# Optimization experiments

Measured on AMD Instinct MI355X. Metric: run time of the kernel, lower is better.

## Reference

```python
import jax, jax.numpy as jnp
import numpy as np

B, QL, HID = 4, 1, 4096
H, KVH, D = 16, 4, 256      # num_heads, num_kv_heads, head_dim
PAST = 8191
S = PAST + QL               # kv_seq_len = 8192
K_KEEP, R = 2048, 128       # heavy-hitter budget, channel top-r
THETA = 10000.0


def _rotate_half(x):
    return jnp.concatenate([-x[..., D // 2:], x[..., :D // 2]], axis=-1)


def _rope_tables(seq_len):
    inv_freq = 1.0 / (THETA ** (jnp.arange(0, D, 2, dtype=jnp.float32) / D))
    t = jnp.arange(seq_len, dtype=jnp.float32)
    freqs = jnp.outer(t, inv_freq)
    emb = jnp.concatenate([freqs, freqs], axis=-1)  # [S, D]
    return jnp.cos(emb), jnp.sin(emb)


def setup_inputs() -> dict:
    key = jax.random.key(0)
    ks = jax.random.split(key, 8)
    w = 0.02
    return {
        "hidden_states": jax.random.normal(ks[0], (B, QL, HID), jnp.float32),
        "attention_mask": jnp.zeros((B, 1, QL, S), jnp.float32),
        "position_ids": jnp.full((B, QL), PAST, jnp.int32),
        "past_key": jax.random.normal(ks[1], (B, KVH, PAST, D), jnp.float32),
        "past_value": jax.random.normal(ks[2], (B, KVH, PAST, D), jnp.float32),
        "Wq": w * jax.random.normal(ks[3], (H * D, HID), jnp.float32),
        "Wk": w * jax.random.normal(ks[4], (KVH * D, HID), jnp.float32),
        "Wv": w * jax.random.normal(ks[5], (KVH * D, HID), jnp.float32),
        "Wo": w * jax.random.normal(ks[6], (HID, H * D), jnp.float32),
    }


def reference(hidden_states, attention_mask, position_ids, past_key, past_value, Wq, Wk, Wv, Wo):
    b, q_len, _ = hidden_states.shape
    # QKV projections (no bias)
    q = (hidden_states @ Wq.T).reshape(b, q_len, H, D).transpose(0, 2, 1, 3)    # [b,H,q,D]
    k = (hidden_states @ Wk.T).reshape(b, q_len, KVH, D).transpose(0, 2, 1, 3)  # [b,KVH,q,D]
    v = (hidden_states @ Wv.T).reshape(b, q_len, KVH, D).transpose(0, 2, 1, 3)

    # RoPE at the current positions
    cos_t, sin_t = _rope_tables(S)
    cos = cos_t[position_ids][:, None]  # [b,1,q,D]
    sin = sin_t[position_ids][:, None]
    q = q * cos + _rotate_half(q) * sin
    k = k * cos + _rotate_half(k) * sin

    # append to KV cache, then GQA repeat (repeat_interleave over head dim)
    key = jnp.concatenate([past_key, k], axis=2)      # [b,KVH,S,D]
    value = jnp.concatenate([past_value, v], axis=2)
    n_rep = H // KVH
    key_r = jnp.repeat(key, n_rep, axis=1)            # [b,H,S,D]
    value_r = jnp.repeat(value, n_rep, axis=1)

    # --- heavy-hitter approximate scores: top-r channels of |q| ---
    i1 = jax.lax.top_k(jnp.abs(q), R)[1]                                   # [b,H,q,R]
    Q_hat = jnp.take_along_axis(q, i1, axis=-1)                            # [b,H,q,R]
    K_hat = jnp.take_along_axis(key_r, jnp.broadcast_to(i1, (b, H, S, R)), axis=-1)  # [b,H,S,R]
    scale = jnp.sqrt(D * jnp.abs(Q_hat).sum(-1, keepdims=True)
                     / jnp.abs(q).sum(-1, keepdims=True))                  # [b,H,q,1]
    s_hat = jax.nn.softmax(jnp.einsum('bhqr,bhsr->bhqs', Q_hat, K_hat) / scale
                           + attention_mask, axis=-1)                      # [b,H,q,S]

    # --- evict all but the top-k heavy hitters (rank of s_hat, descending) ---
    ranks = jnp.argsort(jnp.argsort(-s_hat, axis=-1), axis=-1)             # [b,H,q,S]
    aw = jnp.einsum('bhqd,bhsd->bhqs', q, key_r) / np.sqrt(D).astype(np.float32)
    aw = jnp.where(ranks >= K_KEEP, -jnp.inf, aw) + attention_mask
    probs = jax.nn.softmax(aw, axis=-1)
    y = jnp.einsum('bhqs,bhsd->bhqd', probs, value_r)                      # [b,H,q,D]

    out = y.transpose(0, 2, 1, 3).reshape(b, q_len, H * D) @ Wo.T          # [b,q,HID]
    return out
```

## Files before the change

### kernel.cpp

```cpp
#include <hip/hip_runtime.h>
#include <cmath>

#define B_   4
#define H_   16
#define KVH_ 4
#define D_   256
#define HID_ 4096
#define PAST_ 8191
#define S_   8192
#define KKEEP_ 2048
#define R_   128

#define OFF_Q     0
#define OFF_KN    16384
#define OFF_VN    20480
#define OFF_SCALE 24576
#define OFF_CMASK 24640
#define OFF_F     32768
#define OFF_A     557056
#define OFF_P     1081344
#define OFF_YP    1605632
#define OFF_Y     2654208

__global__ __launch_bounds__(256) void k1_qkv(
    const float* __restrict__ hidden, const int* __restrict__ pos_ids,
    const float* __restrict__ Wq, const float* __restrict__ Wk, const float* __restrict__ Wv,
    float* __restrict__ q_ws, float* __restrict__ knew, float* __restrict__ vnew)
{
    int slot = blockIdx.x >> 7;
    int d    = blockIdx.x & 127;
    const float* W; float* outp; int head; bool rope; int bstride;
    if (slot < 16)      { W = Wq; head = slot;      outp = q_ws + head * D_; rope = true;  bstride = H_ * D_; }
    else if (slot < 20) { W = Wk; head = slot - 16; outp = knew + head * D_; rope = true;  bstride = KVH_ * D_; }
    else                { W = Wv; head = slot - 20; outp = vnew + head * D_; rope = false; bstride = KVH_ * D_; }

    int rowbase = head * D_ + d;
    const float* w0 = W + (size_t)rowbase * HID_;
    const float* w1 = W + (size_t)(rowbase + 128) * HID_;

    float acc0[4] = {0.f, 0.f, 0.f, 0.f};
    float acc1[4] = {0.f, 0.f, 0.f, 0.f};
#pragma unroll
    for (int i = 0; i < 4; ++i) {
        int c = (threadIdx.x + 256 * i) * 4;
        float4 a0 = *(const float4*)(w0 + c);
        float4 a1 = *(const float4*)(w1 + c);
#pragma unroll
        for (int b = 0; b < 4; ++b) {
            float4 hv = *(const float4*)(hidden + b * HID_ + c);
            acc0[b] += a0.x * hv.x + a0.y * hv.y + a0.z * hv.z + a0.w * hv.w;
            acc1[b] += a1.x * hv.x + a1.y * hv.y + a1.z * hv.z + a1.w * hv.w;
        }
    }
#pragma unroll
    for (int off = 1; off < 64; off <<= 1) {
#pragma unroll
        for (int b = 0; b < 4; ++b) {
            acc0[b] += __shfl_xor(acc0[b], off, 64);
            acc1[b] += __shfl_xor(acc1[b], off, 64);
        }
    }
    __shared__ float red[4][8];
    int wv = threadIdx.x >> 6, ln = threadIdx.x & 63;
    if (ln == 0) {
#pragma unroll
        for (int b = 0; b < 4; ++b) { red[wv][b] = acc0[b]; red[wv][4 + b] = acc1[b]; }
    }
    __syncthreads();
    if (threadIdx.x == 0) {
        float x = (float)d * (1.0f / 128.0f);
        float invf = 1.0f / powf(10000.0f, x);
        for (int b = 0; b < 4; ++b) {
            float s0 = red[0][b] + red[1][b] + red[2][b] + red[3][b];
            float s1 = red[0][4 + b] + red[1][4 + b] + red[2][4 + b] + red[3][4 + b];
            float o0, o1;
            if (rope) {
                float ang = (float)pos_ids[b] * invf;
                double ad = (double)ang;
                float c = (float)cos(ad), sn = (float)sin(ad);
                o0 = s0 * c - s1 * sn;
                o1 = s1 * c + s0 * sn;
            } else { o0 = s0; o1 = s1; }
            outp[b * bstride + d]       = o0;
            outp[b * bstride + d + 128] = o1;
        }
    }
}

__global__ __launch_bounds__(256) void k1b_chan(
    const float* __restrict__ q_ws, float* __restrict__ scale_ws, unsigned* __restrict__ cmask_ws)
{
    int bh = blockIdx.x;
    int t  = threadIdx.x;
    __shared__ unsigned ua[256];
    __shared__ float red[256];
    __shared__ unsigned bm[8];
    __shared__ float s_all;

    float qv = q_ws[bh * 256 + t];
    float aq = fabsf(qv);
    ua[t] = __float_as_uint(aq);
    if (t < 8) bm[t] = 0u;
    __syncthreads();

    unsigned mine = ua[t];
    int rank = 0;
    for (int i = 0; i < 256; ++i) {
        unsigned o = ua[i];
        rank += (o > mine) || (o == mine && i < t);
    }
    bool kept = rank < R_;
    if (kept) atomicOr(&bm[t >> 5], 1u << (t & 31));

    red[t] = aq; __syncthreads();
    for (int off = 128; off; off >>= 1) { if (t < off) red[t] += red[t + off]; __syncthreads(); }
    if (t == 0) s_all = red[0];
    __syncthreads();
    red[t] = kept ? aq : 0.f; __syncthreads();
    for (int off = 128; off; off >>= 1) { if (t < off) red[t] += red[t + off]; __syncthreads(); }
    if (t == 0) scale_ws[bh] = sqrtf(256.0f * red[0] / s_all);
    if (t < 8) cmask_ws[bh * 8 + t] = bm[t];
}

__global__ __launch_bounds__(256) void k2_scores(
    const float* __restrict__ past_key, const float* __restrict__ knew,
    const float* __restrict__ q_ws, const float* __restrict__ scale_ws,
    const unsigned* __restrict__ cmask_ws, const float* __restrict__ amask,
    float* __restrict__ fsc, float* __restrict__ asc)
{
    int bkv   = blockIdx.x >> 7;
    int chunk = blockIdx.x & 127;
    int b = bkv >> 2, kvh = bkv & 3;
    int w = threadIdx.x >> 6, lane = threadIdx.x & 63;
    int g = lane >> 4, m = lane & 15;
    int h = kvh * 4 + g;

    const float* qp = q_ws + (b * H_ + h) * D_;
    const unsigned* cm = cmask_ws + (b * H_ + h) * 8;
    float inv_scale = 1.0f / scale_ws[b * H_ + h];

    float qr[16], ar[16];
#pragma unroll
    for (int i = 0; i < 4; ++i)
#pragma unroll
        for (int t = 0; t < 4; ++t) {
            int c = i * 64 + m * 4 + t;
            float q = qp[c];
            qr[i * 4 + t] = q;
            ar[i * 4 + t] = ((cm[c >> 5] >> (c & 31)) & 1u) ? q : 0.f;
        }

    const float* kbase = past_key + (size_t)(b * KVH_ + kvh) * PAST_ * D_;
    const float* knrow = knew + (b * KVH_ + kvh) * D_;
    float* fout = fsc + (size_t)(b * H_ + h) * S_;
    float* aout = asc + (size_t)(b * H_ + h) * S_;
    const float* mrow = amask + b * S_;
    int s0 = chunk * 64 + w * 16;

    const float* rA = (s0     < PAST_) ? (kbase + (size_t)s0 * D_)       : knrow;
    const float* rB = (s0 + 1 < PAST_) ? (kbase + (size_t)(s0 + 1) * D_) : knrow;
    float4 nA0 = *(const float4*)(rA + m * 4);
    float4 nA1 = *(const float4*)(rA + 64 + m * 4);
    float4 nA2 = *(const float4*)(rA + 128 + m * 4);
    float4 nA3 = *(const float4*)(rA + 192 + m * 4);
    float4 nB0 = *(const float4*)(rB + m * 4);
    float4 nB1 = *(const float4*)(rB + 64 + m * 4);
    float4 nB2 = *(const float4*)(rB + 128 + m * 4);
    float4 nB3 = *(const float4*)(rB + 192 + m * 4);

    for (int it = 0; it < 8; ++it) {
        int sA = s0 + 2 * it;
        float4 cA0 = nA0, cA1 = nA1, cA2 = nA2, cA3 = nA3;
        float4 cB0 = nB0, cB1 = nB1, cB2 = nB2, cB3 = nB3;
        if (it < 7) {
            int sn = sA + 2;
            const float* pA = (sn     < PAST_) ? (kbase + (size_t)sn * D_)       : knrow;
            const float* pB = (sn + 1 < PAST_) ? (kbase + (size_t)(sn + 1) * D_) : knrow;
            nA0 = *(const float4*)(pA + m * 4);
            nA1 = *(const float4*)(pA + 64 + m * 4);
            nA2 = *(const float4*)(pA + 128 + m * 4);
            nA3 = *(const float4*)(pA + 192 + m * 4);
            nB0 = *(const float4*)(pB + m * 4);
            nB1 = *(const float4*)(pB + 64 + m * 4);
            nB2 = *(const float4*)(pB + 128 + m * 4);
            nB3 = *(const float4*)(pB + 192 + m * 4);
        }
        float fullA = 0.f, apprA = 0.f, fullB = 0.f, apprB = 0.f;
        fullA += qr[0]*cA0.x + qr[1]*cA0.y + qr[2]*cA0.z + qr[3]*cA0.w;
        apprA += ar[0]*cA0.x + ar[1]*cA0.y + ar[2]*cA0.z + ar[3]*cA0.w;
        fullA += qr[4]*cA1.x + qr[5]*cA1.y + qr[6]*cA1.z + qr[7]*cA1.w;
        apprA += ar[4]*cA1.x + ar[5]*cA1.y + ar[6]*cA1.z + ar[7]*cA1.w;
        fullA += qr[8]*cA2.x + qr[9]*cA2.y + qr[10]*cA2.z + qr[11]*cA2.w;
        apprA += ar[8]*cA2.x + ar[9]*cA2.y + ar[10]*cA2.z + ar[11]*cA2.w;
        fullA += qr[12]*cA3.x + qr[13]*cA3.y + qr[14]*cA3.z + qr[15]*cA3.w;
        apprA += ar[12]*cA3.x + ar[13]*cA3.y + ar[14]*cA3.z + ar[15]*cA3.w;
        fullB += qr[0]*cB0.x + qr[1]*cB0.y + qr[2]*cB0.z + qr[3]*cB0.w;
        apprB += ar[0]*cB0.x + ar[1]*cB0.y + ar[2]*cB0.z + ar[3]*cB0.w;
        fullB += qr[4]*cB1.x + qr[5]*cB1.y + qr[6]*cB1.z + qr[7]*cB1.w;
        apprB += ar[4]*cB1.x + ar[5]*cB1.y + ar[6]*cB1.z + ar[7]*cB1.w;
        fullB += qr[8]*cB2.x + qr[9]*cB2.y + qr[10]*cB2.z + qr[11]*cB2.w;
        apprB += ar[8]*cB2.x + ar[9]*cB2.y + ar[10]*cB2.z + ar[11]*cB2.w;
        fullB += qr[12]*cB3.x + qr[13]*cB3.y + qr[14]*cB3.z + qr[15]*cB3.w;
        apprB += ar[12]*cB3.x + ar[13]*cB3.y + ar[14]*cB3.z + ar[15]*cB3.w;
#pragma unroll
        for (int off = 1; off < 16; off <<= 1) {
            fullA += __shfl_xor(fullA, off, 64);
            apprA += __shfl_xor(apprA, off, 64);
            fullB += __shfl_xor(fullB, off, 64);
            apprB += __shfl_xor(apprB, off, 64);
        }
        float2 mv = *(const float2*)(mrow + sA);
        if (m == 0) {
            float2 o; o.x = fullA * 0.0625f + mv.x; o.y = fullB * 0.0625f + mv.y;
            *(float2*)(fout + sA) = o;
        } else if (m == 1) {
            float2 o; o.x = apprA * inv_scale + mv.x; o.y = apprB * inv_scale + mv.y;
            *(float2*)(aout + sA) = o;
        }
    }
}

#define PAD(s) ((s) + ((s) >> 5))
__global__ __launch_bounds__(1024) void k3_select(
    const float* __restrict__ fsc, const float* __restrict__ asc, float* __restrict__ probs)
{
    int bh = blockIdx.x;
    int t  = threadIdx.x;
    int lane = t & 63, wid = t >> 6;
    __shared__ unsigned ua[8448];
    __shared__ unsigned hist2[16 * 257];
    __shared__ unsigned hist[256];
    __shared__ unsigned sf[256];
    __shared__ int wsum[16], wbase[16];
    __shared__ float wred[16];
    __shared__ unsigned sh_bin; __shared__ int sh_rem;
    __shared__ float sh_M, sh_Z;

    const float* ap = asc + (size_t)bh * S_;
    const float* fp = fsc + (size_t)bh * S_;

#pragma unroll
    for (int i = 0; i < 8; ++i) {
        int s = i * 1024 + t;
        unsigned u = __float_as_uint(ap[s]);
        u ^= (u & 0x80000000u) ? 0xFFFFFFFFu : 0x80000000u;
        ua[PAD(s)] = u;
    }

    unsigned prefix = 0; int rem = KKEEP_;
    for (int pass = 0; pass < 4; ++pass) {
        const int shift = 24 - 8 * pass;
        for (int j = t; j < 16 * 257; j += 1024) hist2[j] = 0;
        __syncthreads();
#pragma unroll
        for (int i = 0; i < 8; ++i) {
            unsigned u = ua[PAD(i * 1024 + t)];
            bool match = (pass == 0) || ((u >> (shift + 8)) == prefix);
            if (match) atomicAdd(&hist2[wid * 257 + ((u >> shift) & 255u)], 1u);
        }
        __syncthreads();
        if (t < 256) {
            unsigned hsum = 0;
#pragma unroll
            for (int w2 = 0; w2 < 16; ++w2) hsum += hist2[w2 * 257 + t];
            hist[t] = hsum;
        }
        __syncthreads();
        if (t < 64) {
            unsigned h0 = hist[t*4], h1 = hist[t*4+1], h2 = hist[t*4+2], h3 = hist[t*4+3];
            unsigned loc = h0 + h1 + h2 + h3;
            unsigned run = loc;
#pragma unroll
            for (int off = 1; off < 64; off <<= 1) {
                unsigned v = __shfl_down(run, off, 64);
                if (t + off < 64) run += v;
            }
            unsigned tail = run - loc;
            sf[t*4+3] = tail + h3;
            sf[t*4+2] = tail + h3 + h2;
            sf[t*4+1] = tail + h3 + h2 + h1;
            sf[t*4+0] = tail + loc;
        }
        __syncthreads();
        if (t < 256) {
            unsigned above = (t == 255) ? 0u : sf[t + 1];
            if (sf[t] >= (unsigned)rem && above < (unsigned)rem) {
                sh_bin = (unsigned)t;
                sh_rem = rem - (int)above;
            }
        }
        __syncthreads();
        prefix = (prefix << 8) | sh_bin;
        rem = sh_rem;
        __syncthreads();
    }
    unsigned ut = prefix; int Need = rem;

    int cnt = 0;
#pragma unroll
    for (int i = 0; i < 8; ++i)
        cnt += (ua[PAD(t * 8 + i)] == ut) ? 1 : 0;
    int inc = cnt;
#pragma unroll
    for (int off = 1; off < 64; off <<= 1) {
        int v = __shfl_up(inc, off, 64);
        if (lane >= off) inc += v;
    }
    if (lane == 63) wsum[wid] = inc;
    __syncthreads();
    if (t == 0) {
        int run = 0;
#pragma unroll
        for (int j = 0; j < 16; ++j) { int c = wsum[j]; wbase[j] = run; run += c; }
    }
    __syncthreads();
    int eqb = wbase[wid] + inc - cnt;
#pragma unroll
    for (int i = 0; i < 8; ++i) {
        int s = t * 8 + i;
        if (ua[PAD(s)] == ut) {
            ua[PAD(s)] = (eqb < Need) ? 0xFFFFFFFFu : 0u;
            ++eqb;
        }
    }
    __syncthreads();

    float m = -3.4e38f, z = 0.f;
#pragma unroll
    for (int i = 0; i < 8; ++i) {
        int s = i * 1024 + t;
        if (ua[PAD(s)] > ut) {
            float f = fp[s];
            if (f > m) { z = z * expf(m - f) + 1.f; m = f; }
            else       { z += expf(f - m); }
        }
    }
    float wm = m;
#pragma unroll
    for (int off = 1; off < 64; off <<= 1) wm = fmaxf(wm, __shfl_xor(wm, off, 64));
    if (lane == 0) wred[wid] = wm;
    __syncthreads();
    if (t == 0) {
        float M = wred[0];
#pragma unroll
        for (int j = 1; j < 16; ++j) M = fmaxf(M, wred[j]);
        sh_M = M;
    }
    __syncthreads();
    float M = sh_M;
    float zs = z * expf(m - M);
#pragma unroll
    for (int off = 1; off < 64; off <<= 1) zs += __shfl_xor(zs, off, 64);
    if (lane == 0) wred[wid] = zs;
    __syncthreads();
    if (t == 0) {
        float Z = 0.f;
#pragma unroll
        for (int j = 0; j < 16; ++j) Z += wred[j];
        sh_Z = Z;
    }
    __syncthreads();
    float invZ = 1.0f / sh_Z;

    float* pp = probs + (size_t)bh * S_;
#pragma unroll
    for (int i = 0; i < 8; ++i) {
        int s = i * 1024 + t;
        pp[s] = (ua[PAD(s)] > ut) ? expf(fp[s] - M) * invZ : 0.f;
    }
}

__global__ __launch_bounds__(256) void k4_wv(
    const float* __restrict__ past_value, const float* __restrict__ vnew,
    const float* __restrict__ probs, float* __restrict__ ypart)
{
    int bkv = blockIdx.x >> 6, chunk = blockIdx.x & 63;
    int b = bkv >> 2, kvh = bkv & 3;
    int w = threadIdx.x >> 6, lane = threadIdx.x & 63;
    int h0 = kvh * 4;

    const float* p0 = probs + (size_t)(b * H_ + h0) * S_;
    const float* vbase = past_value + (size_t)(b * KVH_ + kvh) * PAST_ * D_;
    const float* vnrow = vnew + (b * KVH_ + kvh) * D_;

    float acc[4][4] = {{0.f}};
    int s0 = chunk * 128 + w * 32;

    const float* rA = (s0     < PAST_) ? (vbase + (size_t)s0 * D_)       : vnrow;
    const float* rB = (s0 + 1 < PAST_) ? (vbase + (size_t)(s0 + 1) * D_) : vnrow;
    float4 vnA = *(const float4*)(rA + lane * 4);
    float4 vnB = *(const float4*)(rB + lane * 4);
    float2 pn0 = *(const float2*)(p0 + s0);
    float2 pn1 = *(const float2*)(p0 + S_ + s0);
    float2 pn2 = *(const float2*)(p0 + 2 * S_ + s0);
    float2 pn3 = *(const float2*)(p0 + 3 * S_ + s0);

    for (int it = 0; it < 16; ++it) {
        float4 vA = vnA, vB = vnB;
        float2 c0 = pn0, c1 = pn1, c2 = pn2, c3 = pn3;
        if (it < 15) {
            int sn = s0 + 2 * it + 2;
            const float* pA = (sn     < PAST_) ? (vbase + (size_t)sn * D_)       : vnrow;
            const float* pB = (sn + 1 < PAST_) ? (vbase + (size_t)(sn + 1) * D_) : vnrow;
            vnA = *(const float4*)(pA + lane * 4);
            vnB = *(const float4*)(pB + lane * 4);
            pn0 = *(const float2*)(p0 + sn);
            pn1 = *(const float2*)(p0 + S_ + sn);
            pn2 = *(const float2*)(p0 + 2 * S_ + sn);
            pn3 = *(const float2*)(p0 + 3 * S_ + sn);
        }
        acc[0][0] += c0.x * vA.x + c0.y * vB.x;
        acc[0][1] += c0.x * vA.y + c0.y * vB.y;
        acc[0][2] += c0.x * vA.z + c0.y * vB.z;
        acc[0][3] += c0.x * vA.w + c0.y * vB.w;
        acc[1][0] += c1.x * vA.x + c1.y * vB.x;
        acc[1][1] += c1.x * vA.y + c1.y * vB.y;
        acc[1][2] += c1.x * vA.z + c1.y * vB.z;
        acc[1][3] += c1.x * vA.w + c1.y * vB.w;
        acc[2][0] += c2.x * vA.x + c2.y * vB.x;
        acc[2][1] += c2.x * vA.y + c2.y * vB.y;
        acc[2][2] += c2.x * vA.z + c2.y * vB.z;
        acc[2][3] += c2.x * vA.w + c2.y * vB.w;
        acc[3][0] += c3.x * vA.x + c3.y * vB.x;
        acc[3][1] += c3.x * vA.y + c3.y * vB.y;
        acc[3][2] += c3.x * vA.z + c3.y * vB.z;
        acc[3][3] += c3.x * vA.w + c3.y * vB.w;
    }

    __shared__ float part[4][4][256];
#pragma unroll
    for (int j = 0; j < 4; ++j)
#pragma unroll
        for (int t4 = 0; t4 < 4; ++t4)
            part[w][j][lane * 4 + t4] = acc[j][t4];
    __syncthreads();

    float* yo = ypart + (size_t)(chunk * 16 + bkv) * 1024;
    for (int o = threadIdx.x; o < 1024; o += 256) {
        int j = o >> 8, d = o & 255;
        yo[o] = part[0][j][d] + part[1][j][d] + part[2][j][d] + part[3][j][d];
    }
}

__global__ __launch_bounds__(256) void k5_reduce(const float* __restrict__ ypart, float* __restrict__ yflat)
{
    int bh = blockIdx.x; int b = bh >> 4, h = bh & 15;
    int kvh = h >> 2, j = h & 3;
    int d = threadIdx.x;
    int bkv = b * 4 + kvh;
    float sum = 0.f;
    for (int c = 0; c < 64; ++c)
        sum += ypart[(size_t)(c * 16 + bkv) * 1024 + j * 256 + d];
    yflat[b * 4096 + h * 256 + d] = sum;
}

__global__ __launch_bounds__(256) void k6_out(
    const float* __restrict__ Wo, const float* __restrict__ yflat, float* __restrict__ out)
{
    int i = blockIdx.x;
    const float* wrow = Wo + (size_t)i * HID_;
    float acc[4] = {0.f, 0.f, 0.f, 0.f};
#pragma unroll
    for (int ii = 0; ii < 4; ++ii) {
        int c = (threadIdx.x + 256 * ii) * 4;
        float4 wv = *(const float4*)(wrow + c);
#pragma unroll
        for (int b = 0; b < 4; ++b) {
            float4 yv = *(const float4*)(yflat + b * 4096 + c);
            acc[b] += wv.x * yv.x + wv.y * yv.y + wv.z * yv.z + wv.w * yv.w;
        }
    }
#pragma unroll
    for (int off = 1; off < 64; off <<= 1)
#pragma unroll
        for (int b = 0; b < 4; ++b) acc[b] += __shfl_xor(acc[b], off, 64);
    __shared__ float red[4][4];
    int wv_ = threadIdx.x >> 6, ln = threadIdx.x & 63;
    if (ln == 0)
#pragma unroll
        for (int b = 0; b < 4; ++b) red[wv_][b] = acc[b];
    __syncthreads();
    if (threadIdx.x < 4) {
        int b = threadIdx.x;
        out[b * HID_ + i] = red[0][b] + red[1][b] + red[2][b] + red[3][b];
    }
}

extern "C" void kernel_launch(void* const* d_in, const int* in_sizes, int n_in,
                              void* d_out, int out_size, void* d_ws, size_t ws_size,
                              hipStream_t stream)
{
    const float* hidden = (const float*)d_in[0];
    const float* amask  = (const float*)d_in[1];
    const int*   posids = (const int*)d_in[2];
    const float* pkey   = (const float*)d_in[3];
    const float* pval   = (const float*)d_in[4];
    const float* Wq     = (const float*)d_in[5];
    const float* Wk     = (const float*)d_in[6];
    const float* Wv     = (const float*)d_in[7];
    const float* Wo     = (const float*)d_in[8];
    float* out = (float*)d_out;
    float* ws  = (float*)d_ws;

    float* q_ws   = ws + OFF_Q;
    float* knew   = ws + OFF_KN;
    float* vnew   = ws + OFF_VN;
    float* scale  = ws + OFF_SCALE;
    unsigned* cmask = (unsigned*)(ws + OFF_CMASK);
    float* fsc    = ws + OFF_F;
    float* asc    = ws + OFF_A;
    float* probs  = ws + OFF_P;
    float* ypart  = ws + OFF_YP;
    float* yflat  = ws + OFF_Y;

    k1_qkv  <<<dim3(3072), dim3(256), 0, stream>>>(hidden, posids, Wq, Wk, Wv, q_ws, knew, vnew);
    k1b_chan<<<dim3(64),   dim3(256), 0, stream>>>(q_ws, scale, cmask);
    k2_scores<<<dim3(2048), dim3(256), 0, stream>>>(pkey, knew, q_ws, scale, cmask, amask, fsc, asc);
    k3_select<<<dim3(64),  dim3(1024), 0, stream>>>(fsc, asc, probs);
    k4_wv   <<<dim3(1024), dim3(256), 0, stream>>>(pval, vnew, probs, ypart);
    k5_reduce<<<dim3(64),  dim3(256), 0, stream>>>(ypart, yflat);
    k6_out  <<<dim3(4096), dim3(256), 0, stream>>>(Wo, yflat, out);
}
```

Measured before the change: 427.2 us.

## Gather only kept value rows via compacted index list; precompute RoPE table

The select kernel now writes a per-head bitmask of kept positions. A new compaction kernel unions the masks across the four query heads that share a KV head, builds a prefix-summed index list and compacted probabilities, and pads both to multiples of 128. The weighted-V kernel and the reduce then cover only the compacted rows, skipping value rows whose probability is zero in all four heads. RoPE cos/sin values move out of the per-block QKV path into a tiny separate kernel, at the cost of two extra launches and scattered row gathers.

```diff
diff --git a/kernel.cpp b/kernel.cpp
--- a/kernel.cpp
+++ b/kernel.cpp
@@ -16,14 +16,32 @@
 #define OFF_VN    20480
 #define OFF_SCALE 24576
 #define OFF_CMASK 24640
-#define OFF_F     32768
-#define OFF_A     557056
-#define OFF_P     1081344
-#define OFF_YP    1605632
-#define OFF_Y     2654208
+#define OFF_ROPE  25152
+#define OFF_KBM   26176
+#define OFF_CNT   42560
+#define OFF_F     43008
+#define OFF_A     567296
+#define OFF_P     1091584
+#define OFF_YP    1615872
+#define OFF_PC    OFF_F
+#define OFF_LIST  OFF_A
+#define OFF_Y     OFF_KBM
+
+__global__ __launch_bounds__(256) void k0_rope(const int* __restrict__ pos_ids, float* __restrict__ ropet)
+{
+    for (int e = threadIdx.x; e < 512; e += 256) {
+        int b = e >> 7, d = e & 127;
+        float x = (float)d * (1.0f / 128.0f);
+        float invf = 1.0f / powf(10000.0f, x);
+        float ang = (float)pos_ids[b] * invf;
+        double ad = (double)ang;
+        ropet[e * 2]     = (float)cos(ad);
+        ropet[e * 2 + 1] = (float)sin(ad);
+    }
+}
 
 __global__ __launch_bounds__(256) void k1_qkv(
-    const float* __restrict__ hidden, const int* __restrict__ pos_ids,
+    const float* __restrict__ hidden, const float* __restrict__ ropet,
     const float* __restrict__ Wq, const float* __restrict__ Wk, const float* __restrict__ Wv,
     float* __restrict__ q_ws, float* __restrict__ knew, float* __restrict__ vnew)
 {
@@ -68,16 +86,13 @@
     }
     __syncthreads();
     if (threadIdx.x == 0) {
-        float x = (float)d * (1.0f / 128.0f);
-        float invf = 1.0f / powf(10000.0f, x);
         for (int b = 0; b < 4; ++b) {
             float s0 = red[0][b] + red[1][b] + red[2][b] + red[3][b];
             float s1 = red[0][4 + b] + red[1][4 + b] + red[2][4 + b] + red[3][4 + b];
             float o0, o1;
             if (rope) {
-                float ang = (float)pos_ids[b] * invf;
-                double ad = (double)ang;
-                float c = (float)cos(ad), sn = (float)sin(ad);
+                float c  = ropet[(b * 128 + d) * 2];
+                float sn = ropet[(b * 128 + d) * 2 + 1];
                 o0 = s0 * c - s1 * sn;
                 o1 = s1 * c + s0 * sn;
             } else { o0 = s0; o1 = s1; }
@@ -222,7 +237,8 @@
 
 #define PAD(s) ((s) + ((s) >> 5))
 __global__ __launch_bounds__(1024) void k3_select(
-    const float* __restrict__ fsc, const float* __restrict__ asc, float* __restrict__ probs)
+    const float* __restrict__ fsc, const float* __restrict__ asc,
+    float* __restrict__ probs, unsigned* __restrict__ kbm)
 {
     int bh = blockIdx.x;
     int t  = threadIdx.x;
@@ -363,51 +379,110 @@
     float invZ = 1.0f / sh_Z;
 
     float* pp = probs + (size_t)bh * S_;
+    unsigned* kb = kbm + bh * 256;
 #pragma unroll
     for (int i = 0; i < 8; ++i) {
         int s = i * 1024 + t;
-        pp[s] = (ua[PAD(s)] > ut) ? expf(fp[s] - M) * invZ : 0.f;
-    }
+        bool kp = ua[PAD(s)] > ut;
+        pp[s] = kp ? expf(fp[s] - M) * invZ : 0.f;
+        unsigned long long bal = __ballot(kp);
+        if (lane == 0) {
+            int wd = s >> 5;
+            kb[wd]     = (unsigned)bal;
+            kb[wd + 1] = (unsigned)(bal >> 32);
+        }
+    }
+}
+
+__global__ __launch_bounds__(256) void k3b_compact(
+    const unsigned* __restrict__ kbm, const float* __restrict__ probs,
+    int* __restrict__ counts, int* __restrict__ lst, float* __restrict__ pc)
+{
+    int g = blockIdx.x;
+    int t = threadIdx.x;
+    __shared__ int sc[256];
+
+    unsigned m0 = kbm[(g * 4 + 0) * 256 + t];
+    unsigned m1 = kbm[(g * 4 + 1) * 256 + t];
+    unsigned m2 = kbm[(g * 4 + 2) * 256 + t];
+    unsigned m3 = kbm[(g * 4 + 3) * 256 + t];
+    unsigned u = m0 | m1 | m2 | m3;
+    int cnt = __popc(u);
+    sc[t] = cnt; __syncthreads();
+    for (int off = 1; off < 256; off <<= 1) {
+        int v = (t >= off) ? sc[t - off] : 0;
+        __syncthreads();
+        sc[t] += v;
+        __syncthreads();
+    }
+    int base = sc[t] - cnt;
+    int total = sc[255];
+
+    const float* p0 = probs + (size_t)(g * 4) * S_;
+    int* lg = lst + g * 8192;
+    float* pg = pc + (size_t)g * 4 * 8192;
+#pragma unroll
+    for (int bit = 0; bit < 32; ++bit) {
+        if ((u >> bit) & 1u) {
+            int row = t * 32 + bit;
+            int pos = base + __popc(u & ((1u << bit) - 1u));
+            lg[pos] = row;
+            pg[pos]         = ((m0 >> bit) & 1u) ? p0[row]          : 0.f;
+            pg[8192 + pos]  = ((m1 >> bit) & 1u) ? p0[S_ + row]     : 0.f;
+            pg[16384 + pos] = ((m2 >> bit) & 1u) ? p0[2 * S_ + row] : 0.f;
+            pg[24576 + pos] = ((m3 >> bit) & 1u) ? p0[3 * S_ + row] : 0.f;
+        }
+    }
+    int pad_end = (total + 127) & ~127;
+    for (int p = total + t; p < pad_end; p += 256) {
+        lg[p] = PAST_;
+        pg[p] = 0.f; pg[8192 + p] = 0.f; pg[16384 + p] = 0.f; pg[24576 + p] = 0.f;
+    }
+    if (t == 0) counts[g] = total;
 }
 
 __global__ __launch_bounds__(256) void k4_wv(
     const float* __restrict__ past_value, const float* __restrict__ vnew,
-    const float* __restrict__ probs, float* __restrict__ ypart)
+    const int* __restrict__ counts, const int* __restrict__ lst,
+    const float* __restrict__ pc, float* __restrict__ ypart)
 {
     int bkv = blockIdx.x >> 6, chunk = blockIdx.x & 63;
+    int pad_end = (counts[bkv] + 127) & ~127;
+    if (chunk * 128 >= pad_end) return;
     int b = bkv >> 2, kvh = bkv & 3;
     int w = threadIdx.x >> 6, lane = threadIdx.x & 63;
-    int h0 = kvh * 4;
-
-    const float* p0 = probs + (size_t)(b * H_ + h0) * S_;
+
     const float* vbase = past_value + (size_t)(b * KVH_ + kvh) * PAST_ * D_;
     const float* vnrow = vnew + (b * KVH_ + kvh) * D_;
+    const int* lw = lst + bkv * 8192 + chunk * 128 + w * 32;
+    const float* pw = pc + (size_t)bkv * 4 * 8192 + chunk * 128 + w * 32;
 
     float acc[4][4] = {{0.f}};
-    int s0 = chunk * 128 + w * 32;
-
-    const float* rA = (s0     < PAST_) ? (vbase + (size_t)s0 * D_)       : vnrow;
-    const float* rB = (s0 + 1 < PAST_) ? (vbase + (size_t)(s0 + 1) * D_) : vnrow;
-    float4 vnA = *(const float4*)(rA + lane * 4);
-    float4 vnB = *(const float4*)(rB + lane * 4);
-    float2 pn0 = *(const float2*)(p0 + s0);
-    float2 pn1 = *(const float2*)(p0 + S_ + s0);
-    float2 pn2 = *(const float2*)(p0 + 2 * S_ + s0);
-    float2 pn3 = *(const float2*)(p0 + 3 * S_ + s0);
+
+    int rA = lw[0], rB = lw[1];
+    const float* prA = (rA < PAST_) ? (vbase + (size_t)rA * D_) : vnrow;
+    const float* prB = (rB < PAST_) ? (vbase + (size_t)rB * D_) : vnrow;
+    float4 vnA = *(const float4*)(prA + lane * 4);
+    float4 vnB = *(const float4*)(prB + lane * 4);
+    float2 pn0 = *(const float2*)(pw);
+    float2 pn1 = *(const float2*)(pw + 8192);
+    float2 pn2 = *(const float2*)(pw + 16384);
+    float2 pn3 = *(const float2*)(pw + 24576);
 
     for (int it = 0; it < 16; ++it) {
         float4 vA = vnA, vB = vnB;
         float2 c0 = pn0, c1 = pn1, c2 = pn2, c3 = pn3;
         if (it < 15) {
-            int sn = s0 + 2 * it + 2;
-            const float* pA = (sn     < PAST_) ? (vbase + (size_t)sn * D_)       : vnrow;
-            const float* pB = (sn + 1 < PAST_) ? (vbase + (size_t)(sn + 1) * D_) : vnrow;
+            int p2 = 2 * it + 2;
+            int rA2 = lw[p2], rB2 = lw[p2 + 1];
+            const float* pA = (rA2 < PAST_) ? (vbase + (size_t)rA2 * D_) : vnrow;
+            const float* pB = (rB2 < PAST_) ? (vbase + (size_t)rB2 * D_) : vnrow;
             vnA = *(const float4*)(pA + lane * 4);
             vnB = *(const float4*)(pB + lane * 4);
-            pn0 = *(const float2*)(p0 + sn);
-            pn1 = *(const float2*)(p0 + S_ + sn);
-            pn2 = *(const float2*)(p0 + 2 * S_ + sn);
-            pn3 = *(const float2*)(p0 + 3 * S_ + sn);
+            pn0 = *(const float2*)(pw + p2);
+            pn1 = *(const float2*)(pw + 8192 + p2);
+            pn2 = *(const float2*)(pw + 16384 + p2);
+            pn3 = *(const float2*)(pw + 24576 + p2);
         }
         acc[0][0] += c0.x * vA.x + c0.y * vB.x;
         acc[0][1] += c0.x * vA.y + c0.y * vB.y;
@@ -442,14 +517,16 @@
     }
 }
 
-__global__ __launch_bounds__(256) void k5_reduce(const float* __restrict__ ypart, float* __restrict__ yflat)
+__global__ __launch_bounds__(256) void k5_reduce(
+    const float* __restrict__ ypart, const int* __restrict__ counts, float* __restrict__ yflat)
 {
     int bh = blockIdx.x; int b = bh >> 4, h = bh & 15;
     int kvh = h >> 2, j = h & 3;
     int d = threadIdx.x;
     int bkv = b * 4 + kvh;
+    int pcn = (counts[bkv] + 127) >> 7;
     float sum = 0.f;
-    for (int c = 0; c < 64; ++c)
+    for (int c = 0; c < pcn; ++c)
         sum += ypart[(size_t)(c * 16 + bkv) * 1024 + j * 256 + d];
     yflat[b * 4096 + h * 256 + d] = sum;
 }
@@ -507,17 +584,24 @@
     float* vnew   = ws + OFF_VN;
     float* scale  = ws + OFF_SCALE;
     unsigned* cmask = (unsigned*)(ws + OFF_CMASK);
+    float* ropet  = ws + OFF_ROPE;
+    unsigned* kbm = (unsigned*)(ws + OFF_KBM);
+    int* counts   = (int*)(ws + OFF_CNT);
     float* fsc    = ws + OFF_F;
     float* asc    = ws + OFF_A;
     float* probs  = ws + OFF_P;
     float* ypart  = ws + OFF_YP;
+    float* pc     = ws + OFF_PC;
+    int* lst      = (int*)(ws + OFF_LIST);
     float* yflat  = ws + OFF_Y;
 
-    k1_qkv  <<<dim3(3072), dim3(256), 0, stream>>>(hidden, posids, Wq, Wk, Wv, q_ws, knew, vnew);
+    k0_rope <<<dim3(1),    dim3(256), 0, stream>>>(posids, ropet);
+    k1_qkv  <<<dim3(3072), dim3(256), 0, stream>>>(hidden, ropet, Wq, Wk, Wv, q_ws, knew, vnew);
     k1b_chan<<<dim3(64),   dim3(256), 0, stream>>>(q_ws, scale, cmask);
     k2_scores<<<dim3(2048), dim3(256), 0, stream>>>(pkey, knew, q_ws, scale, cmask, amask, fsc, asc);
-    k3_select<<<dim3(64),  dim3(1024), 0, stream>>>(fsc, asc, probs);
-    k4_wv   <<<dim3(1024), dim3(256), 0, stream>>>(pval, vnew, probs, ypart);
-    k5_reduce<<<dim3(64),  dim3(256), 0, stream>>>(ypart, yflat);
+    k3_select<<<dim3(64),  dim3(1024), 0, stream>>>(fsc, asc, probs, kbm);
+    k3b_compact<<<dim3(16), dim3(256), 0, stream>>>(kbm, probs, counts, lst, pc);
+    k4_wv   <<<dim3(1024), dim3(256), 0, stream>>>(pval, vnew, counts, lst, pc, ypart);
+    k5_reduce<<<dim3(64),  dim3(256), 0, stream>>>(ypart, counts, yflat);
     k6_out  <<<dim3(4096), dim3(256), 0, stream>>>(Wo, yflat, out);
 }
```

New measurement: 474.8 us. 1.11x slower.
